# Performance work log

Measured on AMD Instinct MI355X. Metric: run time of the kernel, lower is better.

## Reference

```python
import jax, jax.numpy as jnp
import numpy as np

B = 4096
INPUT_DIM = 1024
ARG_IN = 8
IN_HIDDEN = 64
OUT_HIDDEN = [4096, 4096, 4096]
NUM_CELL_TYPES = 16
NUM_CLASSES = 10
LN_EPS = 1e-5


def _xavier(key, shape):
    # shape = (..., fan_in, fan_out); xavier uniform like torch init
    fan_in, fan_out = shape[-2], shape[-1]
    lim = float(np.sqrt(6.0 / (fan_in + fan_out)))
    return jax.random.uniform(key, shape, jnp.float32, -lim, lim)


def setup_inputs() -> dict:
    key = jax.random.key(0)
    ks = jax.random.split(key, 12)
    prev = OUT_HIDDEN[0] // ARG_IN  # 512
    inp = {
        "x": jax.random.normal(ks[0], (B, INPUT_DIM), jnp.float32),
        "labels": jax.random.randint(ks[1], (B,), 0, NUM_CLASSES),
        # outer nets (stored as (in, out))
        "Wout0": _xavier(ks[2], (INPUT_DIM, OUT_HIDDEN[0])),
        "bout0": jnp.zeros((OUT_HIDDEN[0],), jnp.float32),
        "Wout1": _xavier(ks[3], (prev, OUT_HIDDEN[1])),
        "bout1": jnp.zeros((OUT_HIDDEN[1],), jnp.float32),
        "Wout2": _xavier(ks[4], (prev, OUT_HIDDEN[2])),
        "bout2": jnp.zeros((OUT_HIDDEN[2],), jnp.float32),
        # per-cell-type inner MLPs, stacked over group dim T
        "W1": _xavier(ks[5], (NUM_CELL_TYPES, ARG_IN, IN_HIDDEN)),
        "b1": jnp.zeros((NUM_CELL_TYPES, IN_HIDDEN), jnp.float32),
        "W2": _xavier(ks[6], (NUM_CELL_TYPES, IN_HIDDEN, IN_HIDDEN)),
        "b2": jnp.zeros((NUM_CELL_TYPES, IN_HIDDEN), jnp.float32),
        "W3": _xavier(ks[7], (NUM_CELL_TYPES, IN_HIDDEN, 1))[..., 0],  # (T, H)
        "b3": jnp.zeros((NUM_CELL_TYPES,), jnp.float32),
        # output head
        "Wfc": _xavier(ks[8], (prev, NUM_CLASSES)),
        "bfc": jnp.zeros((NUM_CLASSES,), jnp.float32),
    }
    return inp


def _layernorm(x):
    mu = jnp.mean(x, axis=-1, keepdims=True)
    var = jnp.var(x, axis=-1, keepdims=True)
    return (x - mu) * jax.lax.rsqrt(var + LN_EPS)


def _inner_mlps(out, W1, b1, W2, b2, W3, b3):
    # out: (B, D) with D = T * Cg * ARG_IN; grouped tiny MLPs, vectorized over T
    bsz = out.shape[0]
    z = out.reshape(bsz, NUM_CELL_TYPES, -1, ARG_IN)  # (B, T, Cg, A)
    h = jax.nn.relu(jnp.einsum("btca,tah->btch", z, W1) + b1[None, :, None, :])
    h = jax.nn.relu(jnp.einsum("btch,thk->btck", h, W2) + b2[None, :, None, :])
    y = jnp.einsum("btch,th->btc", h, W3) + b3[None, :, None]  # (B, T, Cg)
    return y.reshape(bsz, -1)  # (B, T*Cg)


def reference(x, labels, Wout0, bout0, Wout1, bout1, Wout2, bout2,
              W1, b1, W2, b2, W3, b3, Wfc, bfc):
    outs = [(Wout0, bout0), (Wout1, bout1), (Wout2, bout2)]
    out = x.reshape(x.shape[0], -1)
    for W, b in outs:
        out = _layernorm(out @ W + b)
        out = _inner_mlps(out, W1, b1, W2, b2, W3, b3)
        # dropout p=0.0 -> identity
    logits = out @ Wfc + bfc  # (B, num_classes)
    logp = jax.nn.log_softmax(logits, axis=-1)
    loss = -jnp.mean(jnp.take_along_axis(logp, labels[:, None], axis=1))
    return logits, loss
```

## Files before the change

### kernel.cpp

```cpp
#include <hip/hip_runtime.h>
#include <hip/hip_bf16.h>
#include <math.h>

constexpr int BATCH   = 4096;
constexpr int NCLS    = 10;
constexpr int NHID    = 4096;
constexpr int PREV    = 512;
constexpr int NTYPES  = 16;
constexpr int CG      = 32;
constexpr float LN_EPS = 1e-5f;

typedef __attribute__((ext_vector_type(8))) short short8;
typedef __attribute__((ext_vector_type(4))) float f32x4;

__global__ __launch_bounds__(256)
void gemm_mfma_kernel(const __hip_bfloat16* __restrict__ A,
                      const __hip_bfloat16* __restrict__ BT,
                      const float* __restrict__ bias,
                      float* __restrict__ C,
                      int N, int K) {
  __shared__ __hip_bfloat16 As[128 * 32];
  __shared__ __hip_bfloat16 Bs[128 * 32];
  const int tid  = threadIdx.x;
  const int wid  = tid >> 6;
  const int lane = tid & 63;
  const int row0 = blockIdx.y * 128;
  const int col0 = blockIdx.x * 128;
  const int wrow = (wid >> 1) * 64;
  const int wcol = (wid & 1) * 64;

  f32x4 acc[4][4] = {};

  const int sr = wid * 32;
  const int lr = lane >> 2;
  const int lc = (lane & 3) * 8;

  const int fr = lane & 15;
  const int fo = (lane >> 4) * 8;

  for (int k0 = 0; k0 < K; k0 += 32) {
    const __hip_bfloat16* ga0 = A  + (size_t)(row0 + sr +      lr) * K + k0 + lc;
    const __hip_bfloat16* ga1 = A  + (size_t)(row0 + sr + 16 + lr) * K + k0 + lc;
    const __hip_bfloat16* gb0 = BT + (size_t)(col0 + sr +      lr) * K + k0 + lc;
    const __hip_bfloat16* gb1 = BT + (size_t)(col0 + sr + 16 + lr) * K + k0 + lc;
    __builtin_amdgcn_global_load_lds((const __attribute__((address_space(1))) void*)ga0,
                                     (__attribute__((address_space(3))) void*)&As[(sr     ) * 32], 16, 0, 0);
    __builtin_amdgcn_global_load_lds((const __attribute__((address_space(1))) void*)ga1,
                                     (__attribute__((address_space(3))) void*)&As[(sr + 16) * 32], 16, 0, 0);
    __builtin_amdgcn_global_load_lds((const __attribute__((address_space(1))) void*)gb0,
                                     (__attribute__((address_space(3))) void*)&Bs[(sr     ) * 32], 16, 0, 0);
    __builtin_amdgcn_global_load_lds((const __attribute__((address_space(1))) void*)gb1,
                                     (__attribute__((address_space(3))) void*)&Bs[(sr + 16) * 32], 16, 0, 0);
    __syncthreads();

    short8 af[4], bfr[4];
    #pragma unroll
    for (int i = 0; i < 4; ++i)
      af[i] = *reinterpret_cast<const short8*>(&As[(wrow + i * 16 + fr) * 32 + fo]);
    #pragma unroll
    for (int j = 0; j < 4; ++j)
      bfr[j] = *reinterpret_cast<const short8*>(&Bs[(wcol + j * 16 + fr) * 32 + fo]);

    #pragma unroll
    for (int i = 0; i < 4; ++i)
      #pragma unroll
      for (int j = 0; j < 4; ++j)
        acc[i][j] = __builtin_amdgcn_mfma_f32_16x16x32_bf16(af[i], bfr[j], acc[i][j], 0, 0, 0);
    __syncthreads();
  }

  #pragma unroll
  for (int j = 0; j < 4; ++j) {
    const int cc = col0 + wcol + j * 16 + (lane & 15);
    const float bv = bias[cc];
    #pragma unroll
    for (int i = 0; i < 4; ++i) {
      const int rr = row0 + wrow + i * 16 + (lane >> 4) * 4;
      #pragma unroll
      for (int r = 0; r < 4; ++r)
        C[(size_t)(rr + r) * N + cc] = acc[i][j][r] + bv;
    }
  }
}

__global__ __launch_bounds__(256)
void cvt_bf16_kernel(const float* __restrict__ in, __hip_bfloat16* __restrict__ out, int n) {
  const int i = (blockIdx.x * 256 + threadIdx.x) * 4;
  if (i >= n) return;
  const float4 v = *reinterpret_cast<const float4*>(&in[i]);
  __hip_bfloat16 t[4];
  t[0] = __float2bfloat16(v.x); t[1] = __float2bfloat16(v.y);
  t[2] = __float2bfloat16(v.z); t[3] = __float2bfloat16(v.w);
  *reinterpret_cast<ushort4*>(&out[i]) = *reinterpret_cast<const ushort4*>(t);
}

__global__ __launch_bounds__(256)
void transpose_cvt_kernel(const float* __restrict__ W, __hip_bfloat16* __restrict__ WT,
                          int K, int N) {
  __shared__ __hip_bfloat16 tile[64][65];
  const int tid = threadIdx.x;
  const int kt = blockIdx.y * 64, nt = blockIdx.x * 64;
  const int cn = tid & 63;
  for (int r = tid >> 6; r < 64; r += 4)
    tile[cn][r] = __float2bfloat16(W[(size_t)(kt + r) * N + nt + cn]);
  __syncthreads();
  for (int r = tid >> 6; r < 64; r += 4)
    WT[(size_t)(nt + r) * K + kt + cn] = tile[r][cn];
}

__global__ __launch_bounds__(256)
void transpose_w2_bf16_kernel(const float* __restrict__ W2, __hip_bfloat16* __restrict__ W2Tb) {
  const int t = blockIdx.x;
  for (int idx = threadIdx.x; idx < 64 * 64; idx += 256) {
    const int n = idx >> 6, h = idx & 63;
    W2Tb[t * 4096 + n * 64 + h] = __float2bfloat16(W2[t * 4096 + h * 64 + n]);
  }
}

__global__ __launch_bounds__(256)
void ln_stats_kernel(const float* __restrict__ X, float2* __restrict__ stats) {
  const int lane = threadIdx.x & 63;
  const int row  = blockIdx.x * 4 + (threadIdx.x >> 6);
  const float* p = X + (size_t)row * NHID;
  float s = 0.f, ss = 0.f;
  #pragma unroll
  for (int i = 0; i < 16; ++i) {
    const float4 v = *reinterpret_cast<const float4*>(&p[i * 256 + lane * 4]);
    s  += v.x + v.y + v.z + v.w;
    ss += v.x * v.x + v.y * v.y + v.z * v.z + v.w * v.w;
  }
  #pragma unroll
  for (int off = 32; off; off >>= 1) { s += __shfl_xor(s, off); ss += __shfl_xor(ss, off); }
  if (lane == 0) {
    const float mu = s * (1.f / 4096.f);
    float2 st;
    st.x = mu;
    st.y = rsqrtf(ss * (1.f / 4096.f) - mu * mu + LN_EPS);
    stats[row] = st;
  }
}

__global__ __launch_bounds__(256, 2)
void inner_type_kernel(const float* __restrict__ X,
                       const float2* __restrict__ stats,
                       float* __restrict__ out,
                       __hip_bfloat16* __restrict__ outb,
                       const __hip_bfloat16* __restrict__ W2Tb,
                       const float* __restrict__ W1, const float* __restrict__ b1,
                       const float* __restrict__ b2,
                       const float* __restrict__ W3, const float* __restrict__ b3) {
  __shared__ __hip_bfloat16 H1s[128 * 64];
  __shared__ float W1s[512];
  const int tid  = threadIdx.x;
  const int lane = tid & 63;
  const int wvid = tid >> 6;
  const int t    = blockIdx.y;
  const int r0   = blockIdx.x * 64;

  const int fc = lane & 15;
  const int fq = lane >> 4;
  const int rg = tid >> 3;
  const int cg = tid & 7;

  const float* zcol = X + t * 256 + (rg & 7) * 32;

#define LOAD_Z(zr, itv)                                                        \
  {                                                                            \
    const float* zb_ = zcol + (size_t)(r0 + (itv) * 4 + wvid) * NHID;          \
    _Pragma("unroll")                                                          \
    for (int c_ = 0; c_ < 4; ++c_) {                                           \
      *reinterpret_cast<float4*>(&zr[c_ * 8])     =                            \
          *reinterpret_cast<const float4*>(&zb_[c_ * 8]);                      \
      *reinterpret_cast<float4*>(&zr[c_ * 8 + 4]) =                            \
          *reinterpret_cast<const float4*>(&zb_[c_ * 8 + 4]);                  \
    }                                                                          \
  }

  float zA[32], zB[32];
  float2 stA, stB;
  LOAD_Z(zA, 0);
  stA = stats[r0 + wvid];

  W1s[tid]       = W1[t * 512 + tid];
  W1s[256 + tid] = W1[t * 512 + 256 + tid];

  short8 bfrag[4][2];
  #pragma unroll
  for (int cf = 0; cf < 4; ++cf)
    #pragma unroll
    for (int ks = 0; ks < 2; ++ks)
      bfrag[cf][ks] = *reinterpret_cast<const short8*>(
          &W2Tb[(size_t)t * 4096 + (cf * 16 + fc) * 64 + ks * 32 + fq * 8]);

  float b2v[4], w3v[4];
  #pragma unroll
  for (int cf = 0; cf < 4; ++cf) {
    b2v[cf] = b2[t * 64 + cf * 16 + fc];
    w3v[cf] = W3[t * 64 + cf * 16 + fc];
  }
  const float yb = b3[t];

  float b1v[8];
  {
    const float4 bv0 = *reinterpret_cast<const float4*>(&b1[t * 64 + cg * 8]);
    const float4 bv1 = *reinterpret_cast<const float4*>(&b1[t * 64 + cg * 8 + 4]);
    b1v[0] = bv0.x; b1v[1] = bv0.y; b1v[2] = bv0.z; b1v[3] = bv0.w;
    b1v[4] = bv1.x; b1v[5] = bv1.y; b1v[6] = bv1.z; b1v[7] = bv1.w;
  }

  __syncthreads();

  float swv[8];
  #pragma unroll
  for (int jj = 0; jj < 8; ++jj) {
    float s = 0.f;
    #pragma unroll
    for (int q = 0; q < 8; ++q) s += W1s[q * 64 + cg * 8 + jj];
    swv[jj] = s;
  }

#define BODY(zr, stv, itv)                                                     \
  {                                                                            \
    const int row_ = r0 + (itv) * 4 + wvid;                                    \
    const float rs_ = stv.y;                                                   \
    const float c1_ = -stv.x * rs_;                                            \
    float bias2[8];                                                            \
    _Pragma("unroll")                                                          \
    for (int jj = 0; jj < 8; ++jj) bias2[jj] = fmaf(c1_, swv[jj], b1v[jj]);    \
    float dot[4][8];                                                           \
    _Pragma("unroll")                                                          \
    for (int rr = 0; rr < 4; ++rr)                                             \
      _Pragma("unroll")                                                        \
      for (int jj = 0; jj < 8; ++jj) dot[rr][jj] = 0.f;                        \
    _Pragma("unroll")                                                          \
    for (int q = 0; q < 8; ++q) {                                              \
      const float4 wa_ = *reinterpret_cast<const float4*>(&W1s[q * 64 + cg * 8]);     \
      const float4 wb_ = *reinterpret_cast<const float4*>(&W1s[q * 64 + cg * 8 + 4]); \
      _Pragma("unroll")                                                        \
      for (int rr = 0; rr < 4; ++rr) {                                         \
        const float zq_ = zr[rr * 8 + q];                                      \
        dot[rr][0] = fmaf(zq_, wa_.x, dot[rr][0]);                             \
        dot[rr][1] = fmaf(zq_, wa_.y, dot[rr][1]);                             \
        dot[rr][2] = fmaf(zq_, wa_.z, dot[rr][2]);                             \
        dot[rr][3] = fmaf(zq_, wa_.w, dot[rr][3]);                             \
        dot[rr][4] = fmaf(zq_, wb_.x, dot[rr][4]);                             \
        dot[rr][5] = fmaf(zq_, wb_.y, dot[rr][5]);                             \
        dot[rr][6] = fmaf(zq_, wb_.z, dot[rr][6]);                             \
        dot[rr][7] = fmaf(zq_, wb_.w, dot[rr][7]);                             \
      }                                                                        \
    }                                                                          \
    _Pragma("unroll")                                                          \
    for (int rr = 0; rr < 4; ++rr) {                                           \
      const int hrow_ = rg * 4 + rr;                                           \
      union { short8 v; __hip_bfloat16 e[8]; } pk_;                            \
      _Pragma("unroll")                                                        \
      for (int jj = 0; jj < 8; ++jj)                                           \
        pk_.e[jj] = __float2bfloat16(                                          \
            fmaxf(fmaf(rs_, dot[rr][jj], bias2[jj]), 0.f));                    \
      const int eo_ = hrow_ * 64 + ((cg * 8) ^ ((hrow_ & 7) << 3));            \
      *reinterpret_cast<short8*>(&H1s[eo_]) = pk_.v;                           \
    }                                                                          \
    f32x4 acc[2][4] = {};                                                      \
    _Pragma("unroll")                                                          \
    for (int ks = 0; ks < 2; ++ks) {                                           \
      short8 a0_, a1_;                                                         \
      {                                                                        \
        const int hrow_ = wvid * 32 + fc;                                      \
        a0_ = *reinterpret_cast<const short8*>(                                \
            &H1s[hrow_ * 64 + ((ks * 32 + fq * 8) ^ ((hrow_ & 7) << 3))]);     \
      }                                                                        \
      {                                                                        \
        const int hrow_ = wvid * 32 + 16 + fc;                                 \
        a1_ = *reinterpret_cast<const short8*>(                                \
            &H1s[hrow_ * 64 + ((ks * 32 + fq * 8) ^ ((hrow_ & 7) << 3))]);     \
      }                                                                        \
      _Pragma("unroll")                                                        \
      for (int cf = 0; cf < 4; ++cf) {                                         \
        acc[0][cf] = __builtin_amdgcn_mfma_f32_16x16x32_bf16(a0_, bfrag[cf][ks], acc[0][cf], 0, 0, 0); \
        acc[1][cf] = __builtin_amdgcn_mfma_f32_16x16x32_bf16(a1_, bfrag[cf][ks], acc[1][cf], 0, 0, 0); \
      }                                                                        \
    }                                                                          \
    float p[2][4];                                                             \
    _Pragma("unroll")                                                          \
    for (int rf = 0; rf < 2; ++rf)                                             \
      _Pragma("unroll")                                                        \
      for (int r = 0; r < 4; ++r) {                                            \
        float s_ = 0.f;                                                        \
        _Pragma("unroll")                                                      \
        for (int cf = 0; cf < 4; ++cf)                                         \
          s_ = fmaf(fmaxf(acc[rf][cf][r] + b2v[cf], 0.f), w3v[cf], s_);        \
        s_ += __shfl_xor(s_, 1);                                               \
        s_ += __shfl_xor(s_, 2);                                               \
        s_ += __shfl_xor(s_, 4);                                               \
        s_ += __shfl_xor(s_, 8);                                               \
        p[rf][r] = s_;                                                         \
      }                                                                        \
    if (fc == 0) {                                                             \
      _Pragma("unroll")                                                        \
      for (int rf = 0; rf < 2; ++rf)                                           \
        _Pragma("unroll")                                                      \
        for (int r = 0; r < 4; ++r) {                                          \
          const int c_ = rf * 16 + fq * 4 + r;                                 \
          const float y_ = p[rf][r] + yb;                                      \
          const size_t oidx_ = (size_t)row_ * PREV + t * CG + c_;              \
          if (out) out[oidx_] = y_;                                            \
          outb[oidx_] = __float2bfloat16(y_);                                  \
        }                                                                      \
    }                                                                          \
  }

  #pragma unroll 1
  for (int it2 = 0; it2 < 8; ++it2) {
    const int itA = it2 * 2;
    LOAD_Z(zB, itA + 1);
    stB = stats[r0 + (itA + 1) * 4 + wvid];
    BODY(zA, stA, itA);
    if (it2 < 7) {
      LOAD_Z(zA, itA + 2);
      stA = stats[r0 + (itA + 2) * 4 + wvid];
    }
    BODY(zB, stB, itA + 1);
  }
#undef LOAD_Z
#undef BODY
}

__global__ __launch_bounds__(64)
void head_kernel(const float* __restrict__ Y, const float* __restrict__ Wfc,
                 const float* __restrict__ bfc, const int* __restrict__ labels,
                 float* __restrict__ logits, float* __restrict__ rowloss) {
  const int b = blockIdx.x;
  const int lane = threadIdx.x;
  const float* yr = Y + (size_t)b * PREV;
  float acc[NCLS] = {};
  for (int k = lane; k < PREV; k += 64) {
    const float yv = yr[k];
    #pragma unroll
    for (int cI = 0; cI < NCLS; ++cI) acc[cI] = fmaf(yv, Wfc[k * NCLS + cI], acc[cI]);
  }
  #pragma unroll
  for (int cI = 0; cI < NCLS; ++cI) {
    #pragma unroll
    for (int off = 32; off; off >>= 1) acc[cI] += __shfl_down(acc[cI], off);
  }
  if (lane == 0) {
    float l[NCLS];
    float m = -1e30f;
    #pragma unroll
    for (int cI = 0; cI < NCLS; ++cI) { l[cI] = acc[cI] + bfc[cI]; m = fmaxf(m, l[cI]); }
    float se = 0.f;
    #pragma unroll
    for (int cI = 0; cI < NCLS; ++cI) se += __expf(l[cI] - m);
    const float lse = m + __logf(se);
    #pragma unroll
    for (int cI = 0; cI < NCLS; ++cI) logits[(size_t)b * NCLS + cI] = l[cI];
    const int lab = labels[b];
    float picked = 0.f;
    #pragma unroll
    for (int cI = 0; cI < NCLS; ++cI) picked += (cI == lab) ? l[cI] : 0.f;
    rowloss[b] = lse - picked;
  }
}

__global__ __launch_bounds__(256)
void loss_reduce_kernel(const float* __restrict__ rowloss, float* __restrict__ loss_out) {
  float s = 0.f;
  for (int i = threadIdx.x; i < BATCH; i += 256) s += rowloss[i];
  #pragma unroll
  for (int off = 32; off; off >>= 1) s += __shfl_down(s, off);
  __shared__ float sb[4];
  if ((threadIdx.x & 63) == 0) sb[threadIdx.x >> 6] = s;
  __syncthreads();
  if (threadIdx.x == 0) loss_out[0] = (sb[0] + sb[1] + sb[2] + sb[3]) * (1.f / BATCH);
}

extern "C" void kernel_launch(void* const* d_in, const int* in_sizes, int n_in,
                              void* d_out, int out_size, void* d_ws, size_t ws_size,
                              hipStream_t stream) {
  const float* x      = (const float*)d_in[0];
  const int*   labels = (const int*)  d_in[1];
  const float* Wout0  = (const float*)d_in[2];
  const float* bout0  = (const float*)d_in[3];
  const float* Wout1  = (const float*)d_in[4];
  const float* bout1  = (const float*)d_in[5];
  const float* Wout2  = (const float*)d_in[6];
  const float* bout2  = (const float*)d_in[7];
  const float* W1     = (const float*)d_in[8];
  const float* b1     = (const float*)d_in[9];
  const float* W2     = (const float*)d_in[10];
  const float* b2     = (const float*)d_in[11];
  const float* W3     = (const float*)d_in[12];
  const float* b3     = (const float*)d_in[13];
  const float* Wfc    = (const float*)d_in[14];
  const float* bfc    = (const float*)d_in[15];

  char* ws = (char*)d_ws;
  float*          Abuf    = (float*)(ws);
  float*          Ybuf    = (float*)(ws + ((size_t)64 << 20));
  __hip_bfloat16* Ybf     = (__hip_bfloat16*)(ws + ((size_t)72 << 20));
  __hip_bfloat16* xbf     = (__hip_bfloat16*)(ws + ((size_t)76 << 20));
  __hip_bfloat16* WT0     = (__hip_bfloat16*)(ws + ((size_t)84 << 20));
  __hip_bfloat16* WT1     = (__hip_bfloat16*)(ws + ((size_t)92 << 20));
  __hip_bfloat16* WT2     = (__hip_bfloat16*)(ws + ((size_t)96 << 20));
  __hip_bfloat16* W2Tb    = (__hip_bfloat16*)(ws + ((size_t)100 << 20));
  float*          rowloss = (float*)(ws + ((size_t)101 << 20));
  float2*         stats   = (float2*)(ws + ((size_t)101 << 20) + (256 << 10));

  float* logits = (float*)d_out;
  float* loss   = logits + (size_t)BATCH * NCLS;

  cvt_bf16_kernel<<<dim3(BATCH * 1024 / 4 / 256), dim3(256), 0, stream>>>(x, xbf, BATCH * 1024);
  transpose_cvt_kernel<<<dim3(NHID / 64, 1024 / 64), dim3(256), 0, stream>>>(Wout0, WT0, 1024, NHID);
  transpose_cvt_kernel<<<dim3(NHID / 64, PREV / 64), dim3(256), 0, stream>>>(Wout1, WT1, PREV, NHID);
  transpose_cvt_kernel<<<dim3(NHID / 64, PREV / 64), dim3(256), 0, stream>>>(Wout2, WT2, PREV, NHID);
  transpose_w2_bf16_kernel<<<dim3(NTYPES), dim3(256), 0, stream>>>(W2, W2Tb);

  const dim3 ggrid(NHID / 128, BATCH / 128), gblk(256);
  const dim3 sgrid(BATCH / 4), sblk(256);
  const dim3 igrid(BATCH / 64, NTYPES), iblk(256);

  gemm_mfma_kernel<<<ggrid, gblk, 0, stream>>>(xbf, WT0, bout0, Abuf, NHID, 1024);
  ln_stats_kernel<<<sgrid, sblk, 0, stream>>>(Abuf, stats);
  inner_type_kernel<<<igrid, iblk, 0, stream>>>(Abuf, stats, nullptr, Ybf, W2Tb, W1, b1, b2, W3, b3);
  gemm_mfma_kernel<<<ggrid, gblk, 0, stream>>>(Ybf, WT1, bout1, Abuf, NHID, PREV);
  ln_stats_kernel<<<sgrid, sblk, 0, stream>>>(Abuf, stats);
  inner_type_kernel<<<igrid, iblk, 0, stream>>>(Abuf, stats, nullptr, Ybf, W2Tb, W1, b1, b2, W3, b3);
  gemm_mfma_kernel<<<ggrid, gblk, 0, stream>>>(Ybf, WT2, bout2, Abuf, NHID, PREV);
  ln_stats_kernel<<<sgrid, sblk, 0, stream>>>(Abuf, stats);
  inner_type_kernel<<<igrid, iblk, 0, stream>>>(Abuf, stats, Ybuf, Ybf, W2Tb, W1, b1, b2, W3, b3);

  head_kernel<<<dim3(BATCH), dim3(64), 0, stream>>>(Ybuf, Wfc, bfc, labels, logits, rowloss);
  loss_reduce_kernel<<<dim3(1), dim3(256), 0, stream>>>(rowloss, loss);
}
```

Before: 414.5 us.

## Compute inner-MLP first layer with bf16 MFMA instead of scalar FMAs

The first 8->64 layer of each per-type inner MLP now runs as MFMA 16x16x32 bf16 instructions, using zero-padded K (only lanes with fq==0 load z and W1 fragments). The W1 transpose to bf16 and the column sums used for the LayerNorm fold move into the one-time weight prep kernel, which removes the W1 shared-memory tile and a __syncthreads. The aim is to cut VALU FMA work and register pressure in the inner kernel. In exchange, three quarters of each MFMA is wasted on padding, and z and W1 are rounded to bf16 before the first layer, which reduces precision.

```diff
diff --git a/kernel.cpp b/kernel.cpp
--- a/kernel.cpp
+++ b/kernel.cpp
@@ -109,11 +109,24 @@
 }
 
 __global__ __launch_bounds__(256)
-void transpose_w2_bf16_kernel(const float* __restrict__ W2, __hip_bfloat16* __restrict__ W2Tb) {
+void prep_weights_kernel(const float* __restrict__ W2, const float* __restrict__ W1,
+                         __hip_bfloat16* __restrict__ W2Tb,
+                         __hip_bfloat16* __restrict__ W1b,
+                         float* __restrict__ swsum) {
   const int t = blockIdx.x;
   for (int idx = threadIdx.x; idx < 64 * 64; idx += 256) {
     const int n = idx >> 6, h = idx & 63;
     W2Tb[t * 4096 + n * 64 + h] = __float2bfloat16(W2[t * 4096 + h * 64 + n]);
+  }
+  for (int idx = threadIdx.x; idx < 512; idx += 256) {
+    const int n = idx >> 3, k = idx & 7;
+    W1b[t * 512 + idx] = __float2bfloat16(W1[t * 512 + k * 64 + n]);
+  }
+  if (threadIdx.x < 64) {
+    float s = 0.f;
+    #pragma unroll
+    for (int k = 0; k < 8; ++k) s += W1[t * 512 + k * 64 + threadIdx.x];
+    swsum[t * 64 + threadIdx.x] = s;
   }
 }
 
@@ -146,43 +159,47 @@
                        float* __restrict__ out,
                        __hip_bfloat16* __restrict__ outb,
                        const __hip_bfloat16* __restrict__ W2Tb,
-                       const float* __restrict__ W1, const float* __restrict__ b1,
+                       const __hip_bfloat16* __restrict__ W1b,
+                       const float* __restrict__ swsum,
+                       const float* __restrict__ b1,
                        const float* __restrict__ b2,
                        const float* __restrict__ W3, const float* __restrict__ b3) {
   __shared__ __hip_bfloat16 H1s[128 * 64];
-  __shared__ float W1s[512];
   const int tid  = threadIdx.x;
   const int lane = tid & 63;
   const int wvid = tid >> 6;
   const int t    = blockIdx.y;
   const int r0   = blockIdx.x * 64;
 
-  const int fc = lane & 15;
-  const int fq = lane >> 4;
-  const int rg = tid >> 3;
-  const int cg = tid & 7;
-
-  const float* zcol = X + t * 256 + (rg & 7) * 32;
+  const int fc  = lane & 15;
+  const int fq  = lane >> 4;
+  const bool ld = (fq == 0);
+
+  const float* zcol = X + t * 256 + fc * 8;
 
 #define LOAD_Z(zr, itv)                                                        \
-  {                                                                            \
+  if (ld) {                                                                    \
     const float* zb_ = zcol + (size_t)(r0 + (itv) * 4 + wvid) * NHID;          \
-    _Pragma("unroll")                                                          \
-    for (int c_ = 0; c_ < 4; ++c_) {                                           \
-      *reinterpret_cast<float4*>(&zr[c_ * 8])     =                            \
-          *reinterpret_cast<const float4*>(&zb_[c_ * 8]);                      \
-      *reinterpret_cast<float4*>(&zr[c_ * 8 + 4]) =                            \
-          *reinterpret_cast<const float4*>(&zb_[c_ * 8 + 4]);                  \
-    }                                                                          \
-  }
-
-  float zA[32], zB[32];
+    *reinterpret_cast<float4*>(&zr[0])  = *reinterpret_cast<const float4*>(zb_);          \
+    *reinterpret_cast<float4*>(&zr[4])  = *reinterpret_cast<const float4*>(zb_ + 4);      \
+    *reinterpret_cast<float4*>(&zr[8])  = *reinterpret_cast<const float4*>(zb_ + 128);    \
+    *reinterpret_cast<float4*>(&zr[12]) = *reinterpret_cast<const float4*>(zb_ + 132);    \
+  }
+
+  float zA[16], zB[16];
+  #pragma unroll
+  for (int i = 0; i < 16; ++i) { zA[i] = 0.f; zB[i] = 0.f; }
   float2 stA, stB;
   LOAD_Z(zA, 0);
   stA = stats[r0 + wvid];
 
-  W1s[tid]       = W1[t * 512 + tid];
-  W1s[256 + tid] = W1[t * 512 + 256 + tid];
+  short8 w1frag[4];
+  #pragma unroll
+  for (int nf = 0; nf < 4; ++nf) {
+    short8 v = {};
+    if (ld) v = *reinterpret_cast<const short8*>(&W1b[(size_t)t * 512 + (nf * 16 + fc) * 8]);
+    w1frag[nf] = v;
+  }
 
   short8 bfrag[4][2];
   #pragma unroll
@@ -192,6 +209,13 @@
       bfrag[cf][ks] = *reinterpret_cast<const short8*>(
           &W2Tb[(size_t)t * 4096 + (cf * 16 + fc) * 64 + ks * 32 + fq * 8]);
 
+  float4 b1q[4], swq[4];
+  #pragma unroll
+  for (int nf = 0; nf < 4; ++nf) {
+    b1q[nf] = *reinterpret_cast<const float4*>(&b1[t * 64 + nf * 16 + fq * 4]);
+    swq[nf] = *reinterpret_cast<const float4*>(&swsum[t * 64 + nf * 16 + fq * 4]);
+  }
+
   float b2v[4], w3v[4];
   #pragma unroll
   for (int cf = 0; cf < 4; ++cf) {
@@ -199,67 +223,50 @@
     w3v[cf] = W3[t * 64 + cf * 16 + fc];
   }
   const float yb = b3[t];
-
-  float b1v[8];
-  {
-    const float4 bv0 = *reinterpret_cast<const float4*>(&b1[t * 64 + cg * 8]);
-    const float4 bv1 = *reinterpret_cast<const float4*>(&b1[t * 64 + cg * 8 + 4]);
-    b1v[0] = bv0.x; b1v[1] = bv0.y; b1v[2] = bv0.z; b1v[3] = bv0.w;
-    b1v[4] = bv1.x; b1v[5] = bv1.y; b1v[6] = bv1.z; b1v[7] = bv1.w;
-  }
-
-  __syncthreads();
-
-  float swv[8];
-  #pragma unroll
-  for (int jj = 0; jj < 8; ++jj) {
-    float s = 0.f;
-    #pragma unroll
-    for (int q = 0; q < 8; ++q) s += W1s[q * 64 + cg * 8 + jj];
-    swv[jj] = s;
-  }
 
 #define BODY(zr, stv, itv)                                                     \
   {                                                                            \
     const int row_ = r0 + (itv) * 4 + wvid;                                    \
     const float rs_ = stv.y;                                                   \
     const float c1_ = -stv.x * rs_;                                            \
-    float bias2[8];                                                            \
+            \
+    short8 zf[2];                                                              \
+    {                                                                          \
+      union { short8 v; __hip_bfloat16 e[8]; } p0, p1;                         \
+      _Pragma("unroll")                                                        \
+      for (int q = 0; q < 8; ++q) {                                            \
+        p0.e[q] = __float2bfloat16(zr[q]);                                     \
+        p1.e[q] = __float2bfloat16(zr[8 + q]);                                 \
+      }                                                                        \
+      zf[0] = p0.v; zf[1] = p1.v;                                              \
+    }                                                                          \
+                  \
+    f32x4 pC[4][2] = {};                                                       \
     _Pragma("unroll")                                                          \
-    for (int jj = 0; jj < 8; ++jj) bias2[jj] = fmaf(c1_, swv[jj], b1v[jj]);    \
-    float dot[4][8];                                                           \
+    for (int nf = 0; nf < 4; ++nf) {                                           \
+      pC[nf][0] = __builtin_amdgcn_mfma_f32_16x16x32_bf16(w1frag[nf], zf[0], pC[nf][0], 0, 0, 0); \
+      pC[nf][1] = __builtin_amdgcn_mfma_f32_16x16x32_bf16(w1frag[nf], zf[1], pC[nf][1], 0, 0, 0); \
+    }                                                                          \
+        \
     _Pragma("unroll")                                                          \
-    for (int rr = 0; rr < 4; ++rr)                                             \
+    for (int nf = 0; nf < 4; ++nf) {                                           \
+      const float bx = fmaf(c1_, swq[nf].x, b1q[nf].x);                        \
+      const float by = fmaf(c1_, swq[nf].y, b1q[nf].y);                        \
+      const float bz = fmaf(c1_, swq[nf].z, b1q[nf].z);                        \
+      const float bw = fmaf(c1_, swq[nf].w, b1q[nf].w);                        \
       _Pragma("unroll")                                                        \
-      for (int jj = 0; jj < 8; ++jj) dot[rr][jj] = 0.f;                        \
-    _Pragma("unroll")                                                          \
-    for (int q = 0; q < 8; ++q) {                                              \
-      const float4 wa_ = *reinterpret_cast<const float4*>(&W1s[q * 64 + cg * 8]);     \
-      const float4 wb_ = *reinterpret_cast<const float4*>(&W1s[q * 64 + cg * 8 + 4]); \
-      _Pragma("unroll")                                                        \
-      for (int rr = 0; rr < 4; ++rr) {                                         \
-        const float zq_ = zr[rr * 8 + q];                                      \
-        dot[rr][0] = fmaf(zq_, wa_.x, dot[rr][0]);                             \
-        dot[rr][1] = fmaf(zq_, wa_.y, dot[rr][1]);                             \
-        dot[rr][2] = fmaf(zq_, wa_.z, dot[rr][2]);                             \
-        dot[rr][3] = fmaf(zq_, wa_.w, dot[rr][3]);                             \
-        dot[rr][4] = fmaf(zq_, wb_.x, dot[rr][4]);                             \
-        dot[rr][5] = fmaf(zq_, wb_.y, dot[rr][5]);                             \
-        dot[rr][6] = fmaf(zq_, wb_.z, dot[rr][6]);                             \
-        dot[rr][7] = fmaf(zq_, wb_.w, dot[rr][7]);                             \
+      for (int ci = 0; ci < 2; ++ci) {                                         \
+        union { uint2 u; __hip_bfloat16 e[4]; } pk_;                           \
+        pk_.e[0] = __float2bfloat16(fmaxf(fmaf(rs_, pC[nf][ci][0], bx), 0.f)); \
+        pk_.e[1] = __float2bfloat16(fmaxf(fmaf(rs_, pC[nf][ci][1], by), 0.f)); \
+        pk_.e[2] = __float2bfloat16(fmaxf(fmaf(rs_, pC[nf][ci][2], bz), 0.f)); \
+        pk_.e[3] = __float2bfloat16(fmaxf(fmaf(rs_, pC[nf][ci][3], bw), 0.f)); \
+        const int cell_ = wvid * 32 + ci * 16 + fc;                            \
+        const int boff_ = cell_ * 128 + ((nf * 32 + fq * 8) ^ ((cell_ & 7) << 4)); \
+        *reinterpret_cast<uint2*>((char*)H1s + boff_) = pk_.u;                 \
       }                                                                        \
     }                                                                          \
-    _Pragma("unroll")                                                          \
-    for (int rr = 0; rr < 4; ++rr) {                                           \
-      const int hrow_ = rg * 4 + rr;                                           \
-      union { short8 v; __hip_bfloat16 e[8]; } pk_;                            \
-      _Pragma("unroll")                                                        \
-      for (int jj = 0; jj < 8; ++jj)                                           \
-        pk_.e[jj] = __float2bfloat16(                                          \
-            fmaxf(fmaf(rs_, dot[rr][jj], bias2[jj]), 0.f));                    \
-      const int eo_ = hrow_ * 64 + ((cg * 8) ^ ((hrow_ & 7) << 3));            \
-      *reinterpret_cast<short8*>(&H1s[eo_]) = pk_.v;                           \
-    }                                                                          \
+                  \
     f32x4 acc[2][4] = {};                                                      \
     _Pragma("unroll")                                                          \
     for (int ks = 0; ks < 2; ++ks) {                                           \
@@ -280,6 +287,7 @@
         acc[1][cf] = __builtin_amdgcn_mfma_f32_16x16x32_bf16(a1_, bfrag[cf][ks], acc[1][cf], 0, 0, 0); \
       }                                                                        \
     }                                                                          \
+                                                              \
     float p[2][4];                                                             \
     _Pragma("unroll")                                                          \
     for (int rf = 0; rf < 2; ++rf)                                             \
@@ -403,6 +411,8 @@
   __hip_bfloat16* WT1     = (__hip_bfloat16*)(ws + ((size_t)92 << 20));
   __hip_bfloat16* WT2     = (__hip_bfloat16*)(ws + ((size_t)96 << 20));
   __hip_bfloat16* W2Tb    = (__hip_bfloat16*)(ws + ((size_t)100 << 20));
+  __hip_bfloat16* W1b     = (__hip_bfloat16*)(ws + ((size_t)100 << 20) + (128 << 10));
+  float*          swsum   = (float*)(ws + ((size_t)100 << 20) + (192 << 10));
   float*          rowloss = (float*)(ws + ((size_t)101 << 20));
   float2*         stats   = (float2*)(ws + ((size_t)101 << 20) + (256 << 10));
 
@@ -413,7 +423,7 @@
   transpose_cvt_kernel<<<dim3(NHID / 64, 1024 / 64), dim3(256), 0, stream>>>(Wout0, WT0, 1024, NHID);
   transpose_cvt_kernel<<<dim3(NHID / 64, PREV / 64), dim3(256), 0, stream>>>(Wout1, WT1, PREV, NHID);
   transpose_cvt_kernel<<<dim3(NHID / 64, PREV / 64), dim3(256), 0, stream>>>(Wout2, WT2, PREV, NHID);
-  transpose_w2_bf16_kernel<<<dim3(NTYPES), dim3(256), 0, stream>>>(W2, W2Tb);
+  prep_weights_kernel<<<dim3(NTYPES), dim3(256), 0, stream>>>(W2, W1, W2Tb, W1b, swsum);
 
   const dim3 ggrid(NHID / 128, BATCH / 128), gblk(256);
   const dim3 sgrid(BATCH / 4), sblk(256);
@@ -421,13 +431,13 @@
 
   gemm_mfma_kernel<<<ggrid, gblk, 0, stream>>>(xbf, WT0, bout0, Abuf, NHID, 1024);
   ln_stats_kernel<<<sgrid, sblk, 0, stream>>>(Abuf, stats);
-  inner_type_kernel<<<igrid, iblk, 0, stream>>>(Abuf, stats, nullptr, Ybf, W2Tb, W1, b1, b2, W3, b3);
+  inner_type_kernel<<<igrid, iblk, 0, stream>>>(Abuf, stats, nullptr, Ybf, W2Tb, W1b, swsum, b1, b2, W3, b3);
   gemm_mfma_kernel<<<ggrid, gblk, 0, stream>>>(Ybf, WT1, bout1, Abuf, NHID, PREV);
   ln_stats_kernel<<<sgrid, sblk, 0, stream>>>(Abuf, stats);
-  inner_type_kernel<<<igrid, iblk, 0, stream>>>(Abuf, stats, nullptr, Ybf, W2Tb, W1, b1, b2, W3, b3);
+  inner_type_kernel<<<igrid, iblk, 0, stream>>>(Abuf, stats, nullptr, Ybf, W2Tb, W1b, swsum, b1, b2, W3, b3);
   gemm_mfma_kernel<<<ggrid, gblk, 0, stream>>>(Ybf, WT2, bout2, Abuf, NHID, PREV);
   ln_stats_kernel<<<sgrid, sblk, 0, stream>>>(Abuf, stats);
-  inner_type_kernel<<<igrid, iblk, 0, stream>>>(Abuf, stats, Ybuf, Ybf, W2Tb, W1, b1, b2, W3, b3);
+  inner_type_kernel<<<igrid, iblk, 0, stream>>>(Abuf, stats, Ybuf, Ybf, W2Tb, W1b, swsum, b1, b2, W3, b3);
 
   head_kernel<<<dim3(BATCH), dim3(64), 0, stream>>>(Ybuf, Wfc, bfc, labels, logits, rowloss);
   loss_reduce_kernel<<<dim3(1), dim3(256), 0, stream>>>(rowloss, loss);
```

Result: faster. 380.4 us (-8.2%).
